# Kernel optimization log

Hardware: AMD Instinct MI355X
Metric: run time of the kernel (lower is better)

Reference implementation:

```python
import jax, jax.numpy as jnp
import numpy as np

N_NODES = 50000
N_EDGES = 800000
IN_CH, HID_CH, OUT_CH = 128, 256, 128
BN_EPS = 1e-5


def gcn_conv(x, W, b, src, dst):
    """PyG GCNConv: h = x @ W; symmetric normalization with self-loops; scatter-add; + bias."""
    N = x.shape[0]
    h = x @ W  # [N, out_ch]
    # degree including self-loop (all edge weights = 1)
    deg = jax.ops.segment_sum(jnp.ones(src.shape[0], h.dtype), dst, num_segments=N) + 1.0
    dis = jax.lax.rsqrt(deg)  # deg^-1/2
    norm = dis[src] * dis[dst]  # [E]
    agg = jax.ops.segment_sum(h[src] * norm[:, None], dst, num_segments=N)
    # self-loop contribution: norm_ii = dis[i]^2
    return agg + h * (dis * dis)[:, None] + b


def batchnorm_train(x, gamma, beta):
    mu = jnp.mean(x, axis=0)
    var = jnp.mean((x - mu) ** 2, axis=0)  # biased var, as torch BN uses for normalization
    return (x - mu) * jax.lax.rsqrt(var + BN_EPS) * gamma + beta


def setup_inputs() -> dict:
    key = jax.random.key(0)
    ks = jax.random.split(key, 4)
    x = jax.random.normal(ks[0], (N_NODES, IN_CH), dtype=jnp.float32)
    edge_index = jax.random.randint(ks[1], (2, N_EDGES), 0, N_NODES, dtype=jnp.int64 if jax.config.jax_enable_x64 else jnp.int32)
    W1 = jax.random.normal(ks[2], (IN_CH, HID_CH), dtype=jnp.float32) * (1.0 / np.sqrt(IN_CH))
    W2 = jax.random.normal(ks[3], (HID_CH, OUT_CH), dtype=jnp.float32) * (1.0 / np.sqrt(HID_CH))
    return {
        "x": x,
        "edge_index": edge_index,
        "W1": W1,
        "b1": jnp.zeros((HID_CH,), jnp.float32),
        "gamma1": jnp.ones((HID_CH,), jnp.float32),
        "beta1": jnp.zeros((HID_CH,), jnp.float32),
        "W2": W2,
        "b2": jnp.zeros((OUT_CH,), jnp.float32),
    }


def reference(x, edge_index, W1, b1, gamma1, beta1, W2, b2):
    src, dst = edge_index[0], edge_index[1]
    h = gcn_conv(x, W1, b1, src, dst)
    h = jax.nn.relu(batchnorm_train(h, gamma1, beta1))
    # dropout omitted (deterministic eval-style reference)
    return gcn_conv(h, W2, b2, src, dst)
```

## Files before the change

### kernel.cpp

```cpp
#include <hip/hip_runtime.h>

#define N_NODES 50000
#define N_EDGES 800000
#define C_IN 128
#define C_HID 256
#define C_OUT 128
#define BN_EPS 1e-5f

typedef __bf16 v8bf __attribute__((ext_vector_type(8)));
typedef float f32x4 __attribute__((ext_vector_type(4)));
typedef unsigned short u16x8 __attribute__((ext_vector_type(8)));

static __device__ __forceinline__ unsigned short f2bf(float f) {
    unsigned int u = __float_as_uint(f);
    u += 0x7fffu + ((u >> 16) & 1u);
    return (unsigned short)(u >> 16);
}
static __device__ __forceinline__ float bf2f(unsigned short h) {
    return __uint_as_float((unsigned int)h << 16);
}
static __device__ __forceinline__ unsigned int pack2(float a, float b) {
    return (unsigned int)f2bf(a) | ((unsigned int)f2bf(b) << 16);
}
static __device__ __forceinline__ float lo2f(unsigned int u) { return __uint_as_float(u << 16); }
static __device__ __forceinline__ float hi2f(unsigned int u) { return __uint_as_float(u & 0xffff0000u); }

#define DEG_BLOCKS ((N_EDGES + 255) / 256)


__global__ __launch_bounds__(256) void k_deg_wtrans(const int* __restrict__ dst, int* __restrict__ deg,
                                                    int* __restrict__ rank,
                                                    const float* __restrict__ W1, const float* __restrict__ W2,
                                                    unsigned short* __restrict__ WT1, unsigned short* __restrict__ WT2) {
    int bx = blockIdx.x, t = threadIdx.x;
    if (bx < DEG_BLOCKS) {
        int e = bx * 256 + t;
        if (e < N_EDGES) rank[e] = atomicAdd(&deg[dst[e]], 1);
    } else {
        int i = (bx - DEG_BLOCKS) * 256 + t;
        if (i < C_IN * C_HID) {
            int n = i >> 7, k = i & 127;
            WT1[n * C_IN + k] = f2bf(W1[k * C_HID + n]);
        } else {
            int j = i - C_IN * C_HID;
            int n = j >> 8, k = j & 255;
            WT2[n * C_HID + k] = f2bf(W2[k * C_OUT + n]);
        }
    }
}


__global__ __launch_bounds__(512) void k_scan1(const int* __restrict__ deg, int* __restrict__ rs,
                                               int* __restrict__ partial, float* __restrict__ dis) {
    __shared__ int s[512];
    int t = threadIdx.x;
    int i = blockIdx.x * 512 + t;
    int v = (i < N_NODES) ? deg[i] : 0;
    if (i < N_NODES) dis[i] = rsqrtf((float)v + 1.0f);
    s[t] = v;
    __syncthreads();
    for (int off = 1; off < 512; off <<= 1) {
        int tv = (t >= off) ? s[t - off] : 0;
        __syncthreads();
        s[t] += tv;
        __syncthreads();
    }
    if (i < N_NODES) rs[i + 1] = s[t];
    if (t == 511) partial[blockIdx.x] = s[511];
}

__global__ __launch_bounds__(256) void k_scan23(int* __restrict__ rs, const int* __restrict__ partial,
                                                int nb) {
    __shared__ int pre[128];
    __shared__ int wsum[2];
    int t = threadIdx.x;
    int lane = t & 63;
    int pv = 0, v = 0;
    if (t < 128) {
        pv = (t < nb) ? partial[t] : 0;
        v = pv;
#pragma unroll
        for (int off = 1; off < 64; off <<= 1) {
            int u = __shfl_up(v, off);
            if (lane >= off) v += u;
        }
        if (lane == 63) wsum[t >> 6] = v;
    }
    __syncthreads();
    if (t < 128) {
        if (t >= 64) v += wsum[0];
        pre[t] = v - pv;
    }
    __syncthreads();
    int i = blockIdx.x * 256 + t;
    if (i < N_NODES) {
        rs[i + 1] = rs[i + 1] + pre[i >> 9];
    }
    if (i == 0) rs[0] = 0;
}


#define PLACE_BLOCKS ((N_EDGES / 4 + 255) / 256)

__global__ __launch_bounds__(256) void k_place_xscale(const int* __restrict__ src, const int* __restrict__ dst,
                                                      const int* __restrict__ rank, const int* __restrict__ rs,
                                                      int* __restrict__ eidx,
                                                      const float* __restrict__ x, const float* __restrict__ dis,
                                                      unsigned short* __restrict__ xs) {
    int bx = blockIdx.x, t = threadIdx.x;
    if (bx < PLACE_BLOCKS) {
        int q = bx * 256 + t;
        int e = q * 4;
        if (e < N_EDGES) {
            int4 d4 = *(const int4*)&dst[e];
            int4 r4 = *(const int4*)&rank[e];
            int4 s4 = *(const int4*)&src[e];
            eidx[rs[d4.x] + r4.x] = s4.x;
            eidx[rs[d4.y] + r4.y] = s4.y;
            eidx[rs[d4.z] + r4.z] = s4.z;
            eidx[rs[d4.w] + r4.w] = s4.w;
        }
    } else {
        int i = (bx - PLACE_BLOCKS) * 256 + t;
        int node = i >> 4;
        if (node < N_NODES) {
            int g8 = (i & 15) * 8;
            float d = dis[node];
            float4 v0 = *(const float4*)&x[(size_t)node * C_IN + g8];
            float4 v1 = *(const float4*)&x[(size_t)node * C_IN + g8 + 4];
            uint4 o = make_uint4(pack2(v0.x * d, v0.y * d), pack2(v0.z * d, v0.w * d),
                                 pack2(v1.x * d, v1.y * d), pack2(v1.z * d, v1.w * d));
            *(uint4*)&xs[(size_t)node * C_IN + g8] = o;
        }
    }
}


template <bool FINAL>
__global__ __launch_bounds__(256) void k_aggr(const unsigned short* __restrict__ g,
                                              const float* __restrict__ dis, const float* __restrict__ bias,
                                              const int* __restrict__ rs, const int* __restrict__ eidx,
                                              unsigned short* __restrict__ outb, float* __restrict__ outf) {
    int wid = (blockIdx.x * 256 + threadIdx.x) >> 6;
    int lane = threadIdx.x & 63;
    if (wid >= N_NODES) return;
    int slot = lane >> 4;
    int cp = lane & 15;
    int s = rs[wid], e = rs[wid + 1];
    float a0 = 0.f, a1 = 0.f, a2 = 0.f, a3 = 0.f, a4 = 0.f, a5 = 0.f, a6 = 0.f, a7 = 0.f;
    int p = s;
    for (; p + 15 < e; p += 16) {
        int i0 = eidx[p + slot];
        int i1 = eidx[p + 4 + slot];
        int i2 = eidx[p + 8 + slot];
        int i3 = eidx[p + 12 + slot];
        u16x8 v0 = *(const u16x8*)&g[(size_t)i0 * 128 + cp * 8];
        u16x8 v1 = *(const u16x8*)&g[(size_t)i1 * 128 + cp * 8];
        u16x8 v2 = *(const u16x8*)&g[(size_t)i2 * 128 + cp * 8];
        u16x8 v3 = *(const u16x8*)&g[(size_t)i3 * 128 + cp * 8];
        a0 += bf2f(v0[0]) + bf2f(v1[0]) + bf2f(v2[0]) + bf2f(v3[0]);
        a1 += bf2f(v0[1]) + bf2f(v1[1]) + bf2f(v2[1]) + bf2f(v3[1]);
        a2 += bf2f(v0[2]) + bf2f(v1[2]) + bf2f(v2[2]) + bf2f(v3[2]);
        a3 += bf2f(v0[3]) + bf2f(v1[3]) + bf2f(v2[3]) + bf2f(v3[3]);
        a4 += bf2f(v0[4]) + bf2f(v1[4]) + bf2f(v2[4]) + bf2f(v3[4]);
        a5 += bf2f(v0[5]) + bf2f(v1[5]) + bf2f(v2[5]) + bf2f(v3[5]);
        a6 += bf2f(v0[6]) + bf2f(v1[6]) + bf2f(v2[6]) + bf2f(v3[6]);
        a7 += bf2f(v0[7]) + bf2f(v1[7]) + bf2f(v2[7]) + bf2f(v3[7]);
    }
    if (p < e) {
        int last = e - 1;
        int j0 = p + slot;
        int j1 = j0 + 4;
        int j2 = j0 + 8;
        int j3 = j0 + 12;
        float w0 = (j0 <= last) ? 1.f : 0.f;
        float w1 = (j1 <= last) ? 1.f : 0.f;
        float w2 = (j2 <= last) ? 1.f : 0.f;
        float w3 = (j3 <= last) ? 1.f : 0.f;
        j0 = min(j0, last); j1 = min(j1, last); j2 = min(j2, last); j3 = min(j3, last);
        int i0 = eidx[j0];
        int i1 = eidx[j1];
        int i2 = eidx[j2];
        int i3 = eidx[j3];
        u16x8 v0 = *(const u16x8*)&g[(size_t)i0 * 128 + cp * 8];
        u16x8 v1 = *(const u16x8*)&g[(size_t)i1 * 128 + cp * 8];
        u16x8 v2 = *(const u16x8*)&g[(size_t)i2 * 128 + cp * 8];
        u16x8 v3 = *(const u16x8*)&g[(size_t)i3 * 128 + cp * 8];
        a0 = fmaf(w0, bf2f(v0[0]), fmaf(w1, bf2f(v1[0]), fmaf(w2, bf2f(v2[0]), fmaf(w3, bf2f(v3[0]), a0))));
        a1 = fmaf(w0, bf2f(v0[1]), fmaf(w1, bf2f(v1[1]), fmaf(w2, bf2f(v2[1]), fmaf(w3, bf2f(v3[1]), a1))));
        a2 = fmaf(w0, bf2f(v0[2]), fmaf(w1, bf2f(v1[2]), fmaf(w2, bf2f(v2[2]), fmaf(w3, bf2f(v3[2]), a2))));
        a3 = fmaf(w0, bf2f(v0[3]), fmaf(w1, bf2f(v1[3]), fmaf(w2, bf2f(v2[3]), fmaf(w3, bf2f(v3[3]), a3))));
        a4 = fmaf(w0, bf2f(v0[4]), fmaf(w1, bf2f(v1[4]), fmaf(w2, bf2f(v2[4]), fmaf(w3, bf2f(v3[4]), a4))));
        a5 = fmaf(w0, bf2f(v0[5]), fmaf(w1, bf2f(v1[5]), fmaf(w2, bf2f(v2[5]), fmaf(w3, bf2f(v3[5]), a5))));
        a6 = fmaf(w0, bf2f(v0[6]), fmaf(w1, bf2f(v1[6]), fmaf(w2, bf2f(v2[6]), fmaf(w3, bf2f(v3[6]), a6))));
        a7 = fmaf(w0, bf2f(v0[7]), fmaf(w1, bf2f(v1[7]), fmaf(w2, bf2f(v2[7]), fmaf(w3, bf2f(v3[7]), a7))));
    }
    a0 += __shfl_xor(a0, 16); a1 += __shfl_xor(a1, 16); a2 += __shfl_xor(a2, 16); a3 += __shfl_xor(a3, 16);
    a4 += __shfl_xor(a4, 16); a5 += __shfl_xor(a5, 16); a6 += __shfl_xor(a6, 16); a7 += __shfl_xor(a7, 16);
    a0 += __shfl_xor(a0, 32); a1 += __shfl_xor(a1, 32); a2 += __shfl_xor(a2, 32); a3 += __shfl_xor(a3, 32);
    a4 += __shfl_xor(a4, 32); a5 += __shfl_xor(a5, 32); a6 += __shfl_xor(a6, 32); a7 += __shfl_xor(a7, 32);
    if (slot < 2) {
        int ch = cp * 8 + slot * 4;
        float r0 = slot ? a4 : a0, r1 = slot ? a5 : a1, r2 = slot ? a6 : a2, r3 = slot ? a7 : a3;
        ushort4 gi = *(const ushort4*)&g[(size_t)wid * 128 + ch];
        float d = dis[wid];
        if (FINAL) {
            float4 bv = *(const float4*)&bias[ch];
            float4 o = make_float4(fmaf(d, r0 + bf2f(gi.x), bv.x), fmaf(d, r1 + bf2f(gi.y), bv.y),
                                   fmaf(d, r2 + bf2f(gi.z), bv.z), fmaf(d, r3 + bf2f(gi.w), bv.w));
            *(float4*)&outf[(size_t)wid * 128 + ch] = o;
        } else {
            ushort4 z;
            z.x = f2bf(d * (r0 + bf2f(gi.x)));
            z.y = f2bf(d * (r1 + bf2f(gi.y)));
            z.z = f2bf(d * (r2 + bf2f(gi.z)));
            z.w = f2bf(d * (r3 + bf2f(gi.w)));
            *(ushort4*)&outb[(size_t)wid * 128 + ch] = z;
        }
    }
}


template <bool TRANS, int KC>
__global__ __launch_bounds__(256, 2) void k_gemmv(const unsigned short* __restrict__ Ah,
                                                  const unsigned short* __restrict__ BT,
                                                  unsigned short* __restrict__ C,
                                                  const float* __restrict__ dis, const float* __restrict__ bias,
                                                  float* __restrict__ bnsum, float* __restrict__ bnsq,
                                                  const float* __restrict__ gamma, const float* __restrict__ beta,
                                                  int M, int N) {
    constexpr int K = KC * 32;
    constexpr int BP = K + 8;
    __shared__ unsigned short Blds[64 * BP];
    __shared__ float tsc_s[K];
    __shared__ float tof_s[K];

    int t = threadIdx.x;
    int w = t >> 6, lane = t & 63;
    int lm = lane & 15, quad = lane >> 4;
    int col0 = blockIdx.y * 64;

    if (TRANS && t < K) {
        float inv_n = 1.0f / (float)N_NODES;
        float mu = bnsum[t] * inv_n;
        float var = bnsq[t] * inv_n - mu * mu;
        float a = gamma[t] * rsqrtf(var + BN_EPS);
        tsc_s[t] = a;
        tof_s[t] = beta[t] - mu * a;
    }
    constexpr int NLD = 64 * K / 8;
    for (int j = t; j < NLD; j += 256) {
        int n = j / (K / 8);
        int kq = j % (K / 8);
        *(uint4*)&Blds[n * BP + kq * 8] = *(const uint4*)&BT[(size_t)(col0 + n) * K + kq * 8];
    }
    __syncthreads();
    v8bf bfr[4][KC];
#pragma unroll
    for (int in = 0; in < 4; ++in)
#pragma unroll
        for (int kc = 0; kc < KC; ++kc)
            bfr[in][kc] = *(const v8bf*)&Blds[(in * 16 + lm) * BP + kc * 32 + quad * 8];
    __syncthreads();

    unsigned short* Ct = Blds + w * (16 * 80);

    float bias_r[4];
    if (!TRANS) {
#pragma unroll
        for (int in = 0; in < 4; ++in) bias_r[in] = bias[col0 + in * 16 + lm];
    }
    float ss[4] = {0.f, 0.f, 0.f, 0.f}, qq[4] = {0.f, 0.f, 0.f, 0.f};

    int strip0 = (blockIdx.x * 4 + w) * 4;
#pragma unroll
    for (int s = 0; s < 4; ++s) {
        int strip = strip0 + s;
        if (strip * 16 >= M) break;
        int arow = strip * 16 + lm;
        uint4 araw[KC];
#pragma unroll
        for (int kc = 0; kc < KC; ++kc)
            araw[kc] = *(const uint4*)&Ah[(size_t)arow * K + kc * 32 + quad * 8];
        float dqa[4];
        if (TRANS) *(float4*)dqa = *(const float4*)&dis[strip * 16 + quad * 4];
        f32x4 acc[4] = {};
#pragma unroll
        for (int kc = 0; kc < KC; ++kc) {
            v8bf af;
            if (TRANS) {
                int kb2 = kc * 32 + quad * 8;
                float4 s0 = *(const float4*)&tsc_s[kb2];
                float4 s1 = *(const float4*)&tsc_s[kb2 + 4];
                float4 o0 = *(const float4*)&tof_s[kb2];
                float4 o1 = *(const float4*)&tof_s[kb2 + 4];
                uint4 h = araw[kc];
                float f0 = fmaxf(fmaf(lo2f(h.x), s0.x, o0.x), 0.f);
                float f1 = fmaxf(fmaf(hi2f(h.x), s0.y, o0.y), 0.f);
                float f2 = fmaxf(fmaf(lo2f(h.y), s0.z, o0.z), 0.f);
                float f3 = fmaxf(fmaf(hi2f(h.y), s0.w, o0.w), 0.f);
                float f4 = fmaxf(fmaf(lo2f(h.z), s1.x, o1.x), 0.f);
                float f5 = fmaxf(fmaf(hi2f(h.z), s1.y, o1.y), 0.f);
                float f6 = fmaxf(fmaf(lo2f(h.w), s1.z, o1.z), 0.f);
                float f7 = fmaxf(fmaf(hi2f(h.w), s1.w, o1.w), 0.f);
                uint4 pk = make_uint4(pack2(f0, f1), pack2(f2, f3), pack2(f4, f5), pack2(f6, f7));
                af = *(v8bf*)&pk;
            } else {
                af = *(v8bf*)&araw[kc];
            }
#pragma unroll
            for (int in = 0; in < 4; ++in)
                acc[in] = __builtin_amdgcn_mfma_f32_16x16x32_bf16(af, bfr[in][kc], acc[in], 0, 0, 0);
        }
#pragma unroll
        for (int in = 0; in < 4; ++in) {
#pragma unroll
            for (int q = 0; q < 4; ++q) {
                float val = TRANS ? acc[in][q] * dqa[q] : acc[in][q] + bias_r[in];
                unsigned short hb = f2bf(val);
                Ct[(quad * 4 + q) * 80 + in * 16 + lm] = hb;
                if (!TRANS) {
                    float v = bf2f(hb);
                    ss[in] += v;
                    qq[in] = fmaf(v, v, qq[in]);
                }
            }
        }
#pragma unroll
        for (int it = 0; it < 2; ++it) {
            int rl = (lane >> 3) + it * 8;
            uint4 v = *(const uint4*)&Ct[rl * 80 + (lane & 7) * 8];
            *(uint4*)&C[(size_t)(strip * 16 + rl) * N + col0 + (lane & 7) * 8] = v;
        }
    }
    if (!TRANS) {
#pragma unroll
        for (int in = 0; in < 4; ++in) {
            float s = ss[in], q2 = qq[in];
            s += __shfl_xor(s, 16); q2 += __shfl_xor(q2, 16);
            s += __shfl_xor(s, 32); q2 += __shfl_xor(q2, 32);
            if (quad == 0) {
                atomicAdd(&bnsum[col0 + in * 16 + lm], s);
                atomicAdd(&bnsq[col0 + in * 16 + lm], q2);
            }
        }
    }
}


extern "C" void kernel_launch(void* const* d_in, const int* in_sizes, int n_in,
                              void* d_out, int out_size, void* d_ws, size_t ws_size,
                              hipStream_t stream) {
    const float* x      = (const float*)d_in[0];
    const int*   ei     = (const int*)d_in[1];
    const float* W1     = (const float*)d_in[2];
    const float* b1     = (const float*)d_in[3];
    const float* gamma1 = (const float*)d_in[4];
    const float* beta1  = (const float*)d_in[5];
    const float* W2     = (const float*)d_in[6];
    const float* b2     = (const float*)d_in[7];
    const int* srcv = ei;
    const int* dstv = ei + N_EDGES;
    float* out = (float*)d_out;

    char* w = (char*)d_ws;
    size_t off = 0;
    auto alloc = [&](size_t bytes) {
        void* p = w + off;
        off = (off + bytes + 255) & ~(size_t)255;
        return p;
    };
    int*   deg     = (int*)alloc(N_NODES * 4);
    float* bnsum   = (float*)alloc(256 * 4);
    float* bnsq    = (float*)alloc(256 * 4);
    size_t zero_bytes = off;
    float* dis     = (float*)alloc(N_NODES * 4);
    int*   rs      = (int*)alloc((N_NODES + 1) * 4);
    int*   rank    = (int*)alloc((size_t)N_EDGES * 4);
    int*   partial = (int*)alloc(128 * 4);
    int*   eidx    = (int*)alloc((size_t)N_EDGES * 4);
    unsigned short* WT1 = (unsigned short*)alloc((size_t)C_IN * C_HID * 2);
    unsigned short* WT2 = (unsigned short*)alloc((size_t)C_HID * C_OUT * 2);
    unsigned short* xs  = (unsigned short*)alloc((size_t)N_NODES * C_IN * 2);
    unsigned short* P   = (unsigned short*)alloc((size_t)N_NODES * C_IN * 2);
    unsigned short* z1  = (unsigned short*)alloc((size_t)N_NODES * C_HID * 2);
    unsigned short* g2  = (unsigned short*)alloc((size_t)N_NODES * C_OUT * 2);
    (void)ws_size; (void)in_sizes; (void)n_in; (void)out_size;

    (void)hipMemsetAsync(deg, 0, zero_bytes, stream);

    int nb = (N_NODES + 511) / 512;
    k_deg_wtrans<<<DEG_BLOCKS + 256, 256, 0, stream>>>(dstv, deg, rank, W1, W2, WT1, WT2);
    k_scan1<<<nb, 512, 0, stream>>>(deg, rs, partial, dis);
    k_scan23<<<(N_NODES + 255) / 256, 256, 0, stream>>>(rs, partial, nb);
    k_place_xscale<<<PLACE_BLOCKS + (N_NODES * 16 + 255) / 256, 256, 0, stream>>>(
        srcv, dstv, rank, rs, eidx, x, dis, xs);

    k_aggr<false><<<(N_NODES * 64 + 255) / 256, 256, 0, stream>>>(xs, dis, nullptr, rs, eidx, P, nullptr);
    dim3 gg1((N_NODES + 255) / 256, C_HID / 64);
    k_gemmv<false, 4><<<gg1, 256, 0, stream>>>(P, WT1, z1, nullptr, b1, bnsum, bnsq, nullptr, nullptr,
                                               N_NODES, C_HID);

    dim3 gg2((N_NODES + 255) / 256, C_OUT / 64);
    k_gemmv<true, 8><<<gg2, 256, 0, stream>>>(z1, WT2, g2, dis, nullptr, bnsum, bnsq, gamma1, beta1,
                                              N_NODES, C_OUT);
    k_aggr<true><<<(N_NODES * 64 + 255) / 256, 256, 0, stream>>>(g2, dis, b2, rs, eidx, nullptr, out);
}
```

Baseline: 256.3 us.

## Move x bf16 cast into degree kernel and apply source scaling in aggregation

The x-to-bf16 cast no longer waits for the degree scan. It now runs in the first kernel alongside the degree atomics and weight transpose, and the per-source dis scaling moves into the first aggregation as per-edge weights gathered from dis. This takes the x conversion off the critical path after the scan and shrinks the place kernel. In exchange, the first aggregation does an extra scattered dis load per edge and uses FMAs instead of plain adds.

```diff
diff --git a/kernel.cpp b/kernel.cpp
--- a/kernel.cpp
+++ b/kernel.cpp
@@ -26,17 +26,19 @@
 static __device__ __forceinline__ float hi2f(unsigned int u) { return __uint_as_float(u & 0xffff0000u); }
 
 #define DEG_BLOCKS ((N_EDGES + 255) / 256)
+#define CAST_BLOCKS ((N_NODES * 16 + 255) / 256)
 
 
 __global__ __launch_bounds__(256) void k_deg_wtrans(const int* __restrict__ dst, int* __restrict__ deg,
                                                     int* __restrict__ rank,
                                                     const float* __restrict__ W1, const float* __restrict__ W2,
-                                                    unsigned short* __restrict__ WT1, unsigned short* __restrict__ WT2) {
+                                                    unsigned short* __restrict__ WT1, unsigned short* __restrict__ WT2,
+                                                    const float* __restrict__ x, unsigned short* __restrict__ xb) {
     int bx = blockIdx.x, t = threadIdx.x;
     if (bx < DEG_BLOCKS) {
         int e = bx * 256 + t;
         if (e < N_EDGES) rank[e] = atomicAdd(&deg[dst[e]], 1);
-    } else {
+    } else if (bx < DEG_BLOCKS + 256) {
         int i = (bx - DEG_BLOCKS) * 256 + t;
         if (i < C_IN * C_HID) {
             int n = i >> 7, k = i & 127;
@@ -45,6 +47,17 @@
             int j = i - C_IN * C_HID;
             int n = j >> 8, k = j & 255;
             WT2[n * C_HID + k] = f2bf(W2[k * C_OUT + n]);
+        }
+    } else {
+        int i = (bx - DEG_BLOCKS - 256) * 256 + t;
+        int node = i >> 4;
+        if (node < N_NODES) {
+            int g8 = (i & 15) * 8;
+            float4 v0 = *(const float4*)&x[(size_t)node * C_IN + g8];
+            float4 v1 = *(const float4*)&x[(size_t)node * C_IN + g8 + 4];
+            uint4 o = make_uint4(pack2(v0.x, v0.y), pack2(v0.z, v0.w),
+                                 pack2(v1.x, v1.y), pack2(v1.z, v1.w));
+            *(uint4*)&xb[(size_t)node * C_IN + g8] = o;
         }
     }
 }
@@ -102,36 +115,19 @@
 
 #define PLACE_BLOCKS ((N_EDGES / 4 + 255) / 256)
 
-__global__ __launch_bounds__(256) void k_place_xscale(const int* __restrict__ src, const int* __restrict__ dst,
-                                                      const int* __restrict__ rank, const int* __restrict__ rs,
-                                                      int* __restrict__ eidx,
-                                                      const float* __restrict__ x, const float* __restrict__ dis,
-                                                      unsigned short* __restrict__ xs) {
-    int bx = blockIdx.x, t = threadIdx.x;
-    if (bx < PLACE_BLOCKS) {
-        int q = bx * 256 + t;
-        int e = q * 4;
-        if (e < N_EDGES) {
-            int4 d4 = *(const int4*)&dst[e];
-            int4 r4 = *(const int4*)&rank[e];
-            int4 s4 = *(const int4*)&src[e];
-            eidx[rs[d4.x] + r4.x] = s4.x;
-            eidx[rs[d4.y] + r4.y] = s4.y;
-            eidx[rs[d4.z] + r4.z] = s4.z;
-            eidx[rs[d4.w] + r4.w] = s4.w;
-        }
-    } else {
-        int i = (bx - PLACE_BLOCKS) * 256 + t;
-        int node = i >> 4;
-        if (node < N_NODES) {
-            int g8 = (i & 15) * 8;
-            float d = dis[node];
-            float4 v0 = *(const float4*)&x[(size_t)node * C_IN + g8];
-            float4 v1 = *(const float4*)&x[(size_t)node * C_IN + g8 + 4];
-            uint4 o = make_uint4(pack2(v0.x * d, v0.y * d), pack2(v0.z * d, v0.w * d),
-                                 pack2(v1.x * d, v1.y * d), pack2(v1.z * d, v1.w * d));
-            *(uint4*)&xs[(size_t)node * C_IN + g8] = o;
-        }
+__global__ __launch_bounds__(256) void k_place(const int* __restrict__ src, const int* __restrict__ dst,
+                                               const int* __restrict__ rank, const int* __restrict__ rs,
+                                               int* __restrict__ eidx) {
+    int q = blockIdx.x * 256 + threadIdx.x;
+    int e = q * 4;
+    if (e < N_EDGES) {
+        int4 d4 = *(const int4*)&dst[e];
+        int4 r4 = *(const int4*)&rank[e];
+        int4 s4 = *(const int4*)&src[e];
+        eidx[rs[d4.x] + r4.x] = s4.x;
+        eidx[rs[d4.y] + r4.y] = s4.y;
+        eidx[rs[d4.z] + r4.z] = s4.z;
+        eidx[rs[d4.w] + r4.w] = s4.w;
     }
 }
 
@@ -158,14 +154,26 @@
         u16x8 v1 = *(const u16x8*)&g[(size_t)i1 * 128 + cp * 8];
         u16x8 v2 = *(const u16x8*)&g[(size_t)i2 * 128 + cp * 8];
         u16x8 v3 = *(const u16x8*)&g[(size_t)i3 * 128 + cp * 8];
-        a0 += bf2f(v0[0]) + bf2f(v1[0]) + bf2f(v2[0]) + bf2f(v3[0]);
-        a1 += bf2f(v0[1]) + bf2f(v1[1]) + bf2f(v2[1]) + bf2f(v3[1]);
-        a2 += bf2f(v0[2]) + bf2f(v1[2]) + bf2f(v2[2]) + bf2f(v3[2]);
-        a3 += bf2f(v0[3]) + bf2f(v1[3]) + bf2f(v2[3]) + bf2f(v3[3]);
-        a4 += bf2f(v0[4]) + bf2f(v1[4]) + bf2f(v2[4]) + bf2f(v3[4]);
-        a5 += bf2f(v0[5]) + bf2f(v1[5]) + bf2f(v2[5]) + bf2f(v3[5]);
-        a6 += bf2f(v0[6]) + bf2f(v1[6]) + bf2f(v2[6]) + bf2f(v3[6]);
-        a7 += bf2f(v0[7]) + bf2f(v1[7]) + bf2f(v2[7]) + bf2f(v3[7]);
+        if (FINAL) {
+            a0 += bf2f(v0[0]) + bf2f(v1[0]) + bf2f(v2[0]) + bf2f(v3[0]);
+            a1 += bf2f(v0[1]) + bf2f(v1[1]) + bf2f(v2[1]) + bf2f(v3[1]);
+            a2 += bf2f(v0[2]) + bf2f(v1[2]) + bf2f(v2[2]) + bf2f(v3[2]);
+            a3 += bf2f(v0[3]) + bf2f(v1[3]) + bf2f(v2[3]) + bf2f(v3[3]);
+            a4 += bf2f(v0[4]) + bf2f(v1[4]) + bf2f(v2[4]) + bf2f(v3[4]);
+            a5 += bf2f(v0[5]) + bf2f(v1[5]) + bf2f(v2[5]) + bf2f(v3[5]);
+            a6 += bf2f(v0[6]) + bf2f(v1[6]) + bf2f(v2[6]) + bf2f(v3[6]);
+            a7 += bf2f(v0[7]) + bf2f(v1[7]) + bf2f(v2[7]) + bf2f(v3[7]);
+        } else {
+            float w0 = dis[i0], w1 = dis[i1], w2 = dis[i2], w3 = dis[i3];
+            a0 = fmaf(w0, bf2f(v0[0]), fmaf(w1, bf2f(v1[0]), fmaf(w2, bf2f(v2[0]), fmaf(w3, bf2f(v3[0]), a0))));
+            a1 = fmaf(w0, bf2f(v0[1]), fmaf(w1, bf2f(v1[1]), fmaf(w2, bf2f(v2[1]), fmaf(w3, bf2f(v3[1]), a1))));
+            a2 = fmaf(w0, bf2f(v0[2]), fmaf(w1, bf2f(v1[2]), fmaf(w2, bf2f(v2[2]), fmaf(w3, bf2f(v3[2]), a2))));
+            a3 = fmaf(w0, bf2f(v0[3]), fmaf(w1, bf2f(v1[3]), fmaf(w2, bf2f(v2[3]), fmaf(w3, bf2f(v3[3]), a3))));
+            a4 = fmaf(w0, bf2f(v0[4]), fmaf(w1, bf2f(v1[4]), fmaf(w2, bf2f(v2[4]), fmaf(w3, bf2f(v3[4]), a4))));
+            a5 = fmaf(w0, bf2f(v0[5]), fmaf(w1, bf2f(v1[5]), fmaf(w2, bf2f(v2[5]), fmaf(w3, bf2f(v3[5]), a5))));
+            a6 = fmaf(w0, bf2f(v0[6]), fmaf(w1, bf2f(v1[6]), fmaf(w2, bf2f(v2[6]), fmaf(w3, bf2f(v3[6]), a6))));
+            a7 = fmaf(w0, bf2f(v0[7]), fmaf(w1, bf2f(v1[7]), fmaf(w2, bf2f(v2[7]), fmaf(w3, bf2f(v3[7]), a7))));
+        }
     }
     if (p < e) {
         int last = e - 1;
@@ -173,15 +181,19 @@
         int j1 = j0 + 4;
         int j2 = j0 + 8;
         int j3 = j0 + 12;
-        float w0 = (j0 <= last) ? 1.f : 0.f;
-        float w1 = (j1 <= last) ? 1.f : 0.f;
-        float w2 = (j2 <= last) ? 1.f : 0.f;
-        float w3 = (j3 <= last) ? 1.f : 0.f;
+        float m0 = (j0 <= last) ? 1.f : 0.f;
+        float m1 = (j1 <= last) ? 1.f : 0.f;
+        float m2 = (j2 <= last) ? 1.f : 0.f;
+        float m3 = (j3 <= last) ? 1.f : 0.f;
         j0 = min(j0, last); j1 = min(j1, last); j2 = min(j2, last); j3 = min(j3, last);
         int i0 = eidx[j0];
         int i1 = eidx[j1];
         int i2 = eidx[j2];
         int i3 = eidx[j3];
+        float w0 = m0, w1 = m1, w2 = m2, w3 = m3;
+        if (!FINAL) {
+            w0 = m0 * dis[i0]; w1 = m1 * dis[i1]; w2 = m2 * dis[i2]; w3 = m3 * dis[i3];
+        }
         u16x8 v0 = *(const u16x8*)&g[(size_t)i0 * 128 + cp * 8];
         u16x8 v1 = *(const u16x8*)&g[(size_t)i1 * 128 + cp * 8];
         u16x8 v2 = *(const u16x8*)&g[(size_t)i2 * 128 + cp * 8];
@@ -210,11 +222,12 @@
                                    fmaf(d, r2 + bf2f(gi.z), bv.z), fmaf(d, r3 + bf2f(gi.w), bv.w));
             *(float4*)&outf[(size_t)wid * 128 + ch] = o;
         } else {
+            float d2 = d * d;
             ushort4 z;
-            z.x = f2bf(d * (r0 + bf2f(gi.x)));
-            z.y = f2bf(d * (r1 + bf2f(gi.y)));
-            z.z = f2bf(d * (r2 + bf2f(gi.z)));
-            z.w = f2bf(d * (r3 + bf2f(gi.w)));
+            z.x = f2bf(fmaf(d, r0, d2 * bf2f(gi.x)));
+            z.y = f2bf(fmaf(d, r1, d2 * bf2f(gi.y)));
+            z.z = f2bf(fmaf(d, r2, d2 * bf2f(gi.z)));
+            z.w = f2bf(fmaf(d, r3, d2 * bf2f(gi.w)));
             *(ushort4*)&outb[(size_t)wid * 128 + ch] = z;
         }
     }
@@ -381,7 +394,7 @@
     int*   eidx    = (int*)alloc((size_t)N_EDGES * 4);
     unsigned short* WT1 = (unsigned short*)alloc((size_t)C_IN * C_HID * 2);
     unsigned short* WT2 = (unsigned short*)alloc((size_t)C_HID * C_OUT * 2);
-    unsigned short* xs  = (unsigned short*)alloc((size_t)N_NODES * C_IN * 2);
+    unsigned short* xb  = (unsigned short*)alloc((size_t)N_NODES * C_IN * 2);
     unsigned short* P   = (unsigned short*)alloc((size_t)N_NODES * C_IN * 2);
     unsigned short* z1  = (unsigned short*)alloc((size_t)N_NODES * C_HID * 2);
     unsigned short* g2  = (unsigned short*)alloc((size_t)N_NODES * C_OUT * 2);
@@ -390,13 +403,13 @@
     (void)hipMemsetAsync(deg, 0, zero_bytes, stream);
 
     int nb = (N_NODES + 511) / 512;
-    k_deg_wtrans<<<DEG_BLOCKS + 256, 256, 0, stream>>>(dstv, deg, rank, W1, W2, WT1, WT2);
+    k_deg_wtrans<<<DEG_BLOCKS + 256 + CAST_BLOCKS, 256, 0, stream>>>(dstv, deg, rank, W1, W2, WT1, WT2,
+                                                                     x, xb);
     k_scan1<<<nb, 512, 0, stream>>>(deg, rs, partial, dis);
     k_scan23<<<(N_NODES + 255) / 256, 256, 0, stream>>>(rs, partial, nb);
-    k_place_xscale<<<PLACE_BLOCKS + (N_NODES * 16 + 255) / 256, 256, 0, stream>>>(
-        srcv, dstv, rank, rs, eidx, x, dis, xs);
-
-    k_aggr<false><<<(N_NODES * 64 + 255) / 256, 256, 0, stream>>>(xs, dis, nullptr, rs, eidx, P, nullptr);
+    k_place<<<PLACE_BLOCKS, 256, 0, stream>>>(srcv, dstv, rank, rs, eidx);
+
+    k_aggr<false><<<(N_NODES * 64 + 255) / 256, 256, 0, stream>>>(xb, dis, nullptr, rs, eidx, P, nullptr);
     dim3 gg1((N_NODES + 255) / 256, C_HID / 64);
     k_gemmv<false, 4><<<gg1, 256, 0, stream>>>(P, WT1, z1, nullptr, b1, bnsum, bnsq, nullptr, nullptr,
                                                N_NODES, C_HID);
```

New measurement: 250.1 us. 1.02x faster.
